# Kernel optimization log

Measured on AMD Instinct MI355X. Metric: run time of the kernel, lower is better.

## Reference

```python
import jax, jax.numpy as jnp
import numpy as np

B, T, F, H, D = 64, 256, 128, 8, 256
E = F * H          # MHA embed dim = input_dim * feat_dim = 1024
HEADS = 4
HD = E // HEADS


def setup_inputs() -> dict:
    key = jax.random.key(0)
    ks = jax.random.split(key, 12)
    def w(k, shape, fan_in):
        return (jax.random.normal(k, shape, jnp.float32) / np.float32(np.sqrt(fan_in)))
    z = lambda *s: jnp.zeros(s, jnp.float32)
    return {
        "x": jax.random.normal(ks[0], (B, T, F), jnp.float32),
        # input_attn MLP: Linear(F, F//4) -> GELU -> Linear(F//4, F) -> Sigmoid
        "attn_w1": w(ks[1], (F, F // 4), F), "attn_b1": z(F // 4),
        "attn_w2": w(ks[2], (F // 4, F), F // 4), "attn_b2": z(F),
        # bank of F tiny GRUs (input=1, hidden=H), stacked along feature axis
        "W_ih": w(ks[3], (F, 3 * H), 1),        # input weight per feature (input size 1)
        "W_hh": w(ks[4], (F, 3 * H, H), H),
        "b_ih": z(F, 3 * H), "b_hh": z(F, 3 * H),
        # MultiheadAttention(E, 4 heads)
        "in_proj_w": w(ks[5], (E, 3 * E), E), "in_proj_b": z(3 * E),
        "mha_out_w": w(ks[6], (E, E), E), "mha_out_b": z(E),
        # out_proj: Linear(E, D)
        "outp_w": w(ks[7], (E, D), E), "outp_b": z(D),
        # FFN: Linear(D, 2D) -> GELU -> Linear(2D, D)
        "ffn_w1": w(ks[8], (D, 2 * D), D), "ffn_b1": z(2 * D),
        "ffn_w2": w(ks[9], (2 * D, D), 2 * D), "ffn_b2": z(D),
    }


def _forward(x, attn_w1, attn_b1, attn_w2, attn_b2,
             W_ih, W_hh, b_ih, b_hh,
             in_proj_w, in_proj_b, mha_out_w, mha_out_b,
             outp_w, outp_b, ffn_w1, ffn_b1, ffn_w2, ffn_b2):
    gelu = lambda v: jax.nn.gelu(v, approximate=False)
    bs, ts, _ = x.shape
    # feature gating (dropout layers are identity in eval mode)
    input_attn = jax.nn.sigmoid(gelu(x @ attn_w1 + attn_b1) @ attn_w2 + attn_b2)  # [B,T,F]
    xg = x * input_attn

    # fused bank of F independent GRUs (input size 1, hidden H), scanned over time
    def step(h, xt):  # h: [B,F,H], xt: [B,F]
        gi = xt[..., None] * W_ih + b_ih                       # [B,F,3H]
        gh = jnp.einsum('bfh,fgh->bfg', h, W_hh) + b_hh        # [B,F,3H]
        ir, iz, inn = jnp.split(gi, 3, axis=-1)
        hr, hz, hn = jnp.split(gh, 3, axis=-1)
        r = jax.nn.sigmoid(ir + hr)
        zg = jax.nn.sigmoid(iz + hz)
        n = jnp.tanh(inn + r * hn)
        h_new = (1.0 - zg) * n + zg * h
        return h_new, h_new

    h0 = jnp.zeros((bs, F, H), x.dtype)
    _, ys = jax.lax.scan(step, h0, jnp.moveaxis(xg, 1, 0))     # ys: [T,B,F,H]
    out = jnp.moveaxis(ys, 0, 1).reshape(bs, ts, E)            # [B,T,E]

    # self-attention (eval: no dropout)
    qkv = out @ in_proj_w + in_proj_b                          # [B,T,3E]
    q, k, v = jnp.split(qkv, 3, axis=-1)
    hsplit = lambda t: t.reshape(bs, ts, HEADS, HD)
    q, k, v = hsplit(q), hsplit(k), hsplit(v)
    scores = jnp.einsum('bqhd,bkhd->bhqk', q, k) / np.float32(np.sqrt(HD))
    attn = jax.nn.softmax(scores, axis=-1)
    ctx = jnp.einsum('bhqk,bkhd->bqhd', attn, v).reshape(bs, ts, E)
    mha_out = ctx @ mha_out_w + mha_out_b

    h1 = mha_out @ outp_w + outp_b                             # [B,T,D]
    ffn = gelu(h1 @ ffn_w1 + ffn_b1) @ ffn_w2 + ffn_b2
    y = h1 + ffn
    feature_importance = input_attn.sum(-1)                    # [B,T]
    return y, feature_importance, input_attn


def reference(x, attn_w1, attn_b1, attn_w2, attn_b2,
              W_ih, W_hh, b_ih, b_hh,
              in_proj_w, in_proj_b, mha_out_w, mha_out_b,
              outp_w, outp_b, ffn_w1, ffn_b1, ffn_w2, ffn_b2):
    return _forward(x, attn_w1, attn_b1, attn_w2, attn_b2,
                    W_ih, W_hh, b_ih, b_hh,
                    in_proj_w, in_proj_b, mha_out_w, mha_out_b,
                    outp_w, outp_b, ffn_w1, ffn_b1, ffn_w2, ffn_b2)
```

## Files before the change

kernel.cpp:

```cpp
#include <hip/hip_runtime.h>
#include <hip/hip_bf16.h>
#include <math.h>

#define B_  64
#define T_  256
#define F_  128
#define H_  8
#define E_  1024
#define NH_ 4
#define HD_ 256
#define D_  256

#define OFF_Y_  0L
#define OFF_FI_ 4194304L
#define OFF_IA_ 4210688L

typedef unsigned short u16;
typedef unsigned int   u32;
typedef short bf16x8 __attribute__((ext_vector_type(8)));
typedef float f32x4  __attribute__((ext_vector_type(4)));

__device__ __forceinline__ float bf2f(u16 u) {
  union { u32 u; float f; } x; x.u = ((u32)u) << 16; return x.f;
}
__device__ __forceinline__ u16 f2bf(float f) {
  union { float f; u32 u; } x; x.f = f;
  u32 r = (x.u + 0x7fffu + ((x.u >> 16) & 1u)) >> 16;
  return (u16)r;
}
__device__ __forceinline__ float gelu_exact(float v) {
  return 0.5f * v * (1.f + erff(v * 0.70710678118654752f));
}
__device__ __forceinline__ float sigmoidf_(float v) {
  return 1.f / (1.f + __expf(-v));
}
__device__ __forceinline__ float ldv(const void* p, long i, bool isf) {
  return isf ? ((const float*)p)[i] : bf2f(((const u16*)p)[i]);
}
__device__ __forceinline__ void stv(void* p, long i, float v, bool isf) {
  if (isf) ((float*)p)[i] = v;
  else ((u16*)p)[i] = f2bf(v);
}
__device__ __forceinline__ void gld16(void* lds, const void* g) {
  __builtin_amdgcn_global_load_lds(
      (const __attribute__((address_space(1))) u32*)g,
      (__attribute__((address_space(3))) u32*)lds, 16, 0, 0);
}

__global__ void detect_dtype(const u16* __restrict__ x, u32* __restrict__ flag) {
  if (threadIdx.x == 0 && blockIdx.x == 0) {
    int good = 0;
    for (int i = 0; i < 512; ++i) {
      u16 v = x[i];
      int e = (v >> 7) & 0xFF;
      if (v == 0 || (e >= 100 && e <= 140)) ++good;
    }
    *flag = (good >= 450) ? 0u : 1u;
  }
}

__global__ __launch_bounds__(256)
void convert_in(const void* __restrict__ src, u16* __restrict__ dst, int n,
                const u32* __restrict__ flag) {
  const bool isf = (*flag != 0);
  int i = blockIdx.x * 256 + threadIdx.x;
  if (i < n) dst[i] = isf ? f2bf(((const float*)src)[i]) : ((const u16*)src)[i];
}

__global__ void transpose_cvt(const void* __restrict__ in, u16* __restrict__ out,
                              int R, int C, const u32* __restrict__ flag) {
  const bool isf = (*flag != 0);
  __shared__ float t[32][33];
  const int c0 = blockIdx.x * 32, r0 = blockIdx.y * 32;
  const int tx = threadIdx.x, ty = threadIdx.y;
  for (int i = ty; i < 32; i += 8)
    t[i][tx] = ldv(in, (long)(r0 + i) * C + c0 + tx, isf);
  __syncthreads();
  for (int i = ty; i < 32; i += 8)
    out[(long)(c0 + i) * R + r0 + tx] = f2bf(t[tx][i]);
}

__global__ __launch_bounds__(128)
void input_mlp2(const void* __restrict__ x,
                const void* __restrict__ w1, const void* __restrict__ b1,
                const void* __restrict__ w2, const void* __restrict__ b2,
                const u32* __restrict__ flag,
                u16* __restrict__ xg, void* __restrict__ dout) {
  const bool isf = (*flag != 0);
  const long row = blockIdx.x;
  const int tid = threadIdx.x;
  __shared__ float xr[F_];
  __shared__ float hid[32];
  __shared__ float red[2];
  float xv = ldv(x, row * F_ + tid, isf);
  xr[tid] = xv;
  __syncthreads();
  if (tid < 32) {
    float s = ldv(b1, tid, isf);
    for (int f = 0; f < F_; ++f) s += xr[f] * ldv(w1, f * 32 + tid, isf);
    hid[tid] = gelu_exact(s);
  }
  __syncthreads();
  float s = ldv(b2, tid, isf);
  #pragma unroll 8
  for (int j = 0; j < 32; ++j) s += hid[j] * ldv(w2, j * F_ + tid, isf);
  float ia = sigmoidf_(s);
  stv(dout, OFF_IA_ + row * F_ + tid, ia, isf);
  xg[row * F_ + tid] = f2bf(ia * xv);
  float v = ia;
  for (int o = 32; o > 0; o >>= 1) v += __shfl_down(v, o);
  if ((tid & 63) == 0) red[tid >> 6] = v;
  __syncthreads();
  if (tid == 0) stv(dout, OFF_FI_ + row, red[0] + red[1], isf);
}

__global__ __launch_bounds__(256)
void gru_scan4(const u16* __restrict__ xg, const void* __restrict__ W_ih,
               const void* __restrict__ W_hh, const void* __restrict__ b_ih,
               const void* __restrict__ b_hh, const u32* __restrict__ flag,
               u16* __restrict__ gruo) {
  const bool isf = (*flag != 0);
  const int tid = threadIdx.x;
  const int ric = tid >> 3;
  const int j   = tid & 7;
  const int rec = blockIdx.x * 32 + ric;
  const int b = rec >> 7, f = rec & 127;
  __shared__ __align__(16) float hbuf[32][8];
  float whr[8], whz[8], whn[8];
  #pragma unroll
  for (int k = 0; k < 8; ++k) {
    whr[k] = ldv(W_hh, (long)f * 192 + j * 8 + k, isf);
    whz[k] = ldv(W_hh, (long)f * 192 + (8 + j) * 8 + k, isf);
    whn[k] = ldv(W_hh, (long)f * 192 + (16 + j) * 8 + k, isf);
  }
  const float wir = ldv(W_ih, f * 24 + j, isf);
  const float wiz = ldv(W_ih, f * 24 + 8 + j, isf);
  const float win = ldv(W_ih, f * 24 + 16 + j, isf);
  const float cbr = ldv(b_ih, f * 24 + j, isf) + ldv(b_hh, f * 24 + j, isf);
  const float cbz = ldv(b_ih, f * 24 + 8 + j, isf) + ldv(b_hh, f * 24 + 8 + j, isf);
  const float bin_ = ldv(b_ih, f * 24 + 16 + j, isf);
  const float bhn_ = ldv(b_hh, f * 24 + 16 + j, isf);
  float h[8];
  #pragma unroll
  for (int k = 0; k < 8; ++k) h[k] = 0.f;
  const u16* xp = xg + (long)b * T_ * F_ + f;
  u16* op = gruo + (long)b * T_ * E_ + f * 8 + j;
  float xv = bf2f(xp[0]);
  for (int t = 0; t < T_; ++t) {
    float xn = (t + 1 < T_) ? bf2f(xp[(t + 1) * F_]) : 0.f;
    float ar = fmaf(xv, wir, cbr);
    float az = fmaf(xv, wiz, cbz);
    float an = bhn_;
    #pragma unroll
    for (int k = 0; k < 8; ++k) {
      ar = fmaf(h[k], whr[k], ar);
      az = fmaf(h[k], whz[k], az);
      an = fmaf(h[k], whn[k], an);
    }
    const float r = sigmoidf_(ar);
    const float z = sigmoidf_(az);
    const float a = fmaf(r, an, fmaf(xv, win, bin_));
    const float e = __expf(2.f * a);
    const float n = 1.f - 2.f / (e + 1.f);
    const float hn = fmaf(z, h[j] - n, n);
    op[(long)t * E_] = f2bf(hn);
    hbuf[ric][j] = hn;
    f32x4 h0 = *(const f32x4*)&hbuf[ric][0];
    f32x4 h1 = *(const f32x4*)&hbuf[ric][4];
    h[0] = h0[0]; h[1] = h0[1]; h[2] = h0[2]; h[3] = h0[3];
    h[4] = h1[0]; h[5] = h1[1]; h[6] = h1[2]; h[7] = h1[3];
    xv = xn;
  }
}

template <int EPI, int COUT>
__global__ __launch_bounds__(256)
void gemm_bt(const u16* __restrict__ A, int lda,
             const u16* __restrict__ Bp, int ldb,
             void* __restrict__ Cg, int ldc,
             const u16* __restrict__ bias, const u16* __restrict__ resid,
             int K, int nbn, const u32* __restrict__ flag) {
  const bool isf = (*flag != 0);
  const int nwg = gridDim.x;
  const int q8 = nwg >> 3, r8 = nwg & 7;
  const int xcd = blockIdx.x & 7, off = blockIdx.x >> 3;
  const int wg = (xcd < r8) ? xcd * (q8 + 1) + off
                            : r8 * (q8 + 1) + (xcd - r8) * q8 + off;
  const int bn = wg % nbn, bm = wg / nbn;
  const int w = threadIdx.x >> 6, lane = threadIdx.x & 63;
  __shared__ __align__(16) u16 As[128 * 64];
  __shared__ __align__(16) u16 Bs[128 * 64];
  const long m0 = (long)bm * 128, n0 = (long)bn * 128;
  const int wm = w >> 1, wn = w & 1;
  const int lr8 = lane >> 3;
  const int csw = ((lane & 7) ^ (lr8 & 7)) * 8;
  f32x4 acc[4][4] = {};
  const int nk = K >> 6;
  const int lr = lane & 15, lq = lane >> 4;
  for (int kt = 0; kt < nk; ++kt) {
    const int k0 = kt << 6;
    __syncthreads();
    #pragma unroll
    for (int c = 0; c < 4; ++c) {
      const int rb = w * 32 + c * 8;
      gld16((char*)As + rb * 128, A + (m0 + rb + lr8) * (long)lda + k0 + csw);
      gld16((char*)Bs + rb * 128, Bp + (n0 + rb + lr8) * (long)ldb + k0 + csw);
    }
    __syncthreads();
    #pragma unroll
    for (int sub = 0; sub < 2; ++sub) {
      const int ch = sub * 4 + lq;
      const int cof = ((ch ^ (lr & 7)) << 3);
      bf16x8 af[4], bfv[4];
      #pragma unroll
      for (int i = 0; i < 4; ++i)
        af[i] = *(const bf16x8*)&As[(wm * 64 + i * 16 + lr) * 64 + cof];
      #pragma unroll
      for (int i = 0; i < 4; ++i)
        bfv[i] = *(const bf16x8*)&Bs[(wn * 64 + i * 16 + lr) * 64 + cof];
      #pragma unroll
      for (int i = 0; i < 4; ++i) {
        #pragma unroll
        for (int j = 0; j < 4; ++j)
          acc[i][j] = __builtin_amdgcn_mfma_f32_16x16x32_bf16(af[i], bfv[j], acc[i][j], 0, 0, 0);
      }
    }
  }
  const int rq = lq * 4;
  #pragma unroll
  for (int j = 0; j < 4; ++j) {
    const long col = n0 + wn * 64 + j * 16 + lr;
    const float bv = (EPI >= 1) ? bf2f(bias[col]) : 0.f;
    #pragma unroll
    for (int i = 0; i < 4; ++i) {
      const long row0 = m0 + wm * 64 + i * 16 + rq;
      #pragma unroll
      for (int q = 0; q < 4; ++q) {
        const long row = row0 + q;
        float v = acc[i][j][q] + bv;
        if (EPI == 2) v = gelu_exact(v);
        if (EPI == 3) v += bf2f(resid[row * (long)ldc + col]);
        if (COUT) stv(Cg, row * (long)ldc + col, v, isf);
        else ((u16*)Cg)[row * (long)ldc + col] = f2bf(v);
      }
    }
  }
}

__global__ __launch_bounds__(256)
void attn_fused(const u16* __restrict__ qkv, u16* __restrict__ ctx) {
  const int z = blockIdx.y, bb = z >> 2, hh = z & 3;
  const int w = threadIdx.x >> 6, lane = threadIdx.x & 63;
  const int tid = threadIdx.x;
  const long t0 = (long)blockIdx.x * 64;
  __shared__ __align__(16) u16 P1[10240];
  __shared__ __align__(16) u16 Pl[64 * 264];
  __shared__ __align__(16) u16 Vt[256 * 40];
  const u16* qb = qkv + (long)bb * T_ * 3 * E_ + hh * HD_;
  const u16* kb = qb + E_;
  const u16* vb = qb + 2 * E_;
  const int rr = lane >> 2, cc = lane & 3;
  const int lr = lane & 15, lq = lane >> 4, lk = lq * 8;
  f32x4 acc[16] = {};
  for (int kt = 0; kt < 8; ++kt) {
    const int k0 = kt * 32;
    __syncthreads();
    gld16((char*)P1 + w * 16 * 64, qb + (t0 + w * 16 + rr) * (3L * E_) + k0 + cc * 8);
    #pragma unroll
    for (int c = 0; c < 4; ++c) {
      const int rb = w * 64 + c * 16;
      gld16((char*)P1 + 4096 + rb * 64, kb + (long)(rb + rr) * (3L * E_) + k0 + cc * 8);
    }
    __syncthreads();
    bf16x8 aq = *(const bf16x8*)&P1[(w * 16 + lr) * 32 + lk];
    #pragma unroll
    for (int nt = 0; nt < 16; ++nt) {
      bf16x8 bk = *(const bf16x8*)&P1[2048 + (nt * 16 + lr) * 32 + lk];
      acc[nt] = __builtin_amdgcn_mfma_f32_16x16x32_bf16(aq, bk, acc[nt], 0, 0, 0);
    }
  }
  #pragma unroll
  for (int q = 0; q < 4; ++q) {
    float mx = -3.4e38f;
    #pragma unroll
    for (int nt = 0; nt < 16; ++nt) mx = fmaxf(mx, acc[nt][q]);
    mx = fmaxf(mx, __shfl_xor(mx, 1));
    mx = fmaxf(mx, __shfl_xor(mx, 2));
    mx = fmaxf(mx, __shfl_xor(mx, 4));
    mx = fmaxf(mx, __shfl_xor(mx, 8));
    float e[16], sum = 0.f;
    #pragma unroll
    for (int nt = 0; nt < 16; ++nt) {
      e[nt] = __expf((acc[nt][q] - mx) * 0.0625f);
      sum += e[nt];
    }
    sum += __shfl_xor(sum, 1);
    sum += __shfl_xor(sum, 2);
    sum += __shfl_xor(sum, 4);
    sum += __shfl_xor(sum, 8);
    const float inv = 1.f / sum;
    const int rowl = w * 16 + lq * 4 + q;
    #pragma unroll
    for (int nt = 0; nt < 16; ++nt)
      Pl[rowl * 264 + nt * 16 + lr] = f2bf(e[nt] * inv);
  }
  f32x4 acc2[16] = {};
  for (int st = 0; st < 8; ++st) {
    const int s0 = st * 32;
    __syncthreads();
    #pragma unroll
    for (int c = 0; c < 4; ++c) {
      const int rb = w * 8 + c * 2;
      gld16((char*)P1 + rb * 512, vb + (s0 + rb + (lane >> 5)) * (3L * E_) + (lane & 31) * 8);
    }
    __syncthreads();
    u16 col[32];
    #pragma unroll
    for (int si = 0; si < 32; ++si) col[si] = P1[si * 256 + tid];
    #pragma unroll
    for (int cq = 0; cq < 4; ++cq)
      *(uint4*)&Vt[tid * 40 + cq * 8] = *(const uint4*)&col[cq * 8];
    __syncthreads();
    bf16x8 pa = *(const bf16x8*)&Pl[(w * 16 + lr) * 264 + s0 + lk];
    #pragma unroll
    for (int nt = 0; nt < 16; ++nt) {
      bf16x8 bv = *(const bf16x8*)&Vt[(nt * 16 + lr) * 40 + lk];
      acc2[nt] = __builtin_amdgcn_mfma_f32_16x16x32_bf16(pa, bv, acc2[nt], 0, 0, 0);
    }
  }
  const int rq = lq * 4;
  #pragma unroll
  for (int nt = 0; nt < 16; ++nt) {
    const int cold = nt * 16 + lr;
    #pragma unroll
    for (int q = 0; q < 4; ++q) {
      const long row = t0 + w * 16 + rq + q;
      ctx[((long)bb * T_ + row) * E_ + hh * HD_ + cold] = f2bf(acc2[nt][q]);
    }
  }
}

extern "C" void kernel_launch(void* const* d_in, const int* in_sizes, int n_in,
                              void* d_out, int out_size, void* d_ws, size_t ws_size,
                              hipStream_t stream) {
  (void)in_sizes; (void)n_in; (void)out_size; (void)ws_size;
  char* ws = (char*)d_ws;
  u16* BIASA = (u16*)(ws + 0);
  u32* FLAG  = (u32*)(ws + 12288);
  u16* wtI   = (u16*)(ws + 65536);
  u16* wtM   = (u16*)(ws + 6356992);
  u16* wtO   = (u16*)(ws + 8454144);
  u16* wtF1  = (u16*)(ws + 8978432);
  u16* wtF2  = (u16*)(ws + 9240576);
  u16* XG    = (u16*)(ws + 9502720);
  u16* GRUO  = (u16*)(ws + 16777216);
  u16* CTX   = GRUO;
  u16* QKV   = (u16*)(ws + 50331648);
  u16* MHA   = (u16*)(ws + 50331648);
  u16* H1    = (u16*)(ws + 83886080);
  u16* FFH   = (u16*)(ws + 92274688);

  detect_dtype<<<1, 64, 0, stream>>>((const u16*)d_in[0], FLAG);

  convert_in<<<12, 256, 0, stream>>>(d_in[10], BIASA + 0,    3072, FLAG);
  convert_in<<<4,  256, 0, stream>>>(d_in[12], BIASA + 3072, 1024, FLAG);
  convert_in<<<1,  256, 0, stream>>>(d_in[14], BIASA + 4096, 256,  FLAG);
  convert_in<<<2,  256, 0, stream>>>(d_in[16], BIASA + 4352, 512,  FLAG);
  convert_in<<<1,  256, 0, stream>>>(d_in[18], BIASA + 4864, 256,  FLAG);

  dim3 tb(32, 8);
  transpose_cvt<<<dim3(3072 / 32, 1024 / 32), tb, 0, stream>>>(d_in[9],  wtI,  1024, 3072, FLAG);
  transpose_cvt<<<dim3(1024 / 32, 1024 / 32), tb, 0, stream>>>(d_in[11], wtM,  1024, 1024, FLAG);
  transpose_cvt<<<dim3(256 / 32, 1024 / 32),  tb, 0, stream>>>(d_in[13], wtO,  1024, 256,  FLAG);
  transpose_cvt<<<dim3(512 / 32, 256 / 32),   tb, 0, stream>>>(d_in[15], wtF1, 256,  512,  FLAG);
  transpose_cvt<<<dim3(256 / 32, 512 / 32),   tb, 0, stream>>>(d_in[17], wtF2, 512,  256,  FLAG);

  input_mlp2<<<B_ * T_, 128, 0, stream>>>(d_in[0], d_in[1], d_in[2], d_in[3], d_in[4],
                                          FLAG, XG, d_out);
  gru_scan4<<<256, 256, 0, stream>>>(XG, d_in[5], d_in[6], d_in[7], d_in[8], FLAG, GRUO);

  gemm_bt<1, 0><<<dim3(128 * 24, 1), 256, 0, stream>>>(GRUO, 1024, wtI, 1024,
      QKV, 3072, BIASA, nullptr, 1024, 24, FLAG);
  attn_fused<<<dim3(4, B_ * NH_), 256, 0, stream>>>(QKV, CTX);
  gemm_bt<1, 0><<<dim3(128 * 8, 1), 256, 0, stream>>>(CTX, 1024, wtM, 1024,
      MHA, 1024, BIASA + 3072, nullptr, 1024, 8, FLAG);
  gemm_bt<1, 0><<<dim3(128 * 2, 1), 256, 0, stream>>>(MHA, 1024, wtO, 1024,
      H1, 256, BIASA + 4096, nullptr, 1024, 2, FLAG);
  gemm_bt<2, 0><<<dim3(128 * 4, 1), 256, 0, stream>>>(H1, 256, wtF1, 256,
      FFH, 512, BIASA + 4352, nullptr, 256, 4, FLAG);
  gemm_bt<3, 1><<<dim3(128 * 2, 1), 256, 0, stream>>>(FFH, 512, wtF2, 512,
      d_out, 256, BIASA + 4864, H1, 512, 2, FLAG);
}
```

Before: 461.3 us.

## Fuse output projection and FFN into one tail kernel; reorder GEMM tiles

Replaces the three tail GEMMs (out-proj, FFN up with GELU, FFN down with residual) with a single kernel that keeps the 32-row H1 and FFN hidden tiles in shared memory. This avoids writing and re-reading the H1 and FFH intermediates through global memory and removes two launches. The weights in the fused kernel are read directly from global memory without LDS staging. The remaining GEMM drops its XCD-aware tile remap for a simple M-major block order. The input MLP's first layer is also split across all 128 threads with a partial-sum reduction instead of using only 32 threads.

```diff
diff --git a/kernel.cpp b/kernel.cpp
--- a/kernel.cpp
+++ b/kernel.cpp
@@ -90,16 +90,24 @@
   const long row = blockIdx.x;
   const int tid = threadIdx.x;
   __shared__ float xr[F_];
+  __shared__ float hid4[4][32];
   __shared__ float hid[32];
   __shared__ float red[2];
   float xv = ldv(x, row * F_ + tid, isf);
   xr[tid] = xv;
   __syncthreads();
-  if (tid < 32) {
-    float s = ldv(b1, tid, isf);
-    for (int f = 0; f < F_; ++f) s += xr[f] * ldv(w1, f * 32 + tid, isf);
-    hid[tid] = gelu_exact(s);
-  }
+  {
+    const int g = tid & 31, part = tid >> 5;
+    const int f0 = part * 32;
+    float s = 0.f;
+    #pragma unroll 8
+    for (int f = 0; f < 32; ++f) s += xr[f0 + f] * ldv(w1, (long)(f0 + f) * 32 + g, isf);
+    hid4[part][g] = s;
+  }
+  __syncthreads();
+  if (tid < 32)
+    hid[tid] = gelu_exact(ldv(b1, tid, isf) + hid4[0][tid] + hid4[1][tid]
+                          + hid4[2][tid] + hid4[3][tid]);
   __syncthreads();
   float s = ldv(b2, tid, isf);
   #pragma unroll 8
@@ -173,20 +181,14 @@
   }
 }
 
-template <int EPI, int COUT>
+template <int EPI>
 __global__ __launch_bounds__(256)
 void gemm_bt(const u16* __restrict__ A, int lda,
              const u16* __restrict__ Bp, int ldb,
-             void* __restrict__ Cg, int ldc,
-             const u16* __restrict__ bias, const u16* __restrict__ resid,
-             int K, int nbn, const u32* __restrict__ flag) {
-  const bool isf = (*flag != 0);
-  const int nwg = gridDim.x;
-  const int q8 = nwg >> 3, r8 = nwg & 7;
-  const int xcd = blockIdx.x & 7, off = blockIdx.x >> 3;
-  const int wg = (xcd < r8) ? xcd * (q8 + 1) + off
-                            : r8 * (q8 + 1) + (xcd - r8) * q8 + off;
-  const int bn = wg % nbn, bm = wg / nbn;
+             u16* __restrict__ Cg, int ldc,
+             const u16* __restrict__ bias,
+             int K, int nbm) {
+  const int bm = blockIdx.x % nbm, bn = blockIdx.x / nbm;
   const int w = threadIdx.x >> 6, lane = threadIdx.x & 63;
   __shared__ __align__(16) u16 As[128 * 64];
   __shared__ __align__(16) u16 Bs[128 * 64];
@@ -235,15 +237,121 @@
     for (int i = 0; i < 4; ++i) {
       const long row0 = m0 + wm * 64 + i * 16 + rq;
       #pragma unroll
+      for (int q = 0; q < 4; ++q)
+        Cg[(row0 + q) * (long)ldc + col] = f2bf(acc[i][j][q] + bv);
+    }
+  }
+}
+
+__global__ __launch_bounds__(256)
+void fused_tail(const u16* __restrict__ MHA,
+                const u16* __restrict__ wtO, const u16* __restrict__ wtF1,
+                const u16* __restrict__ wtF2,
+                const u16* __restrict__ bO, const u16* __restrict__ bF1,
+                const u16* __restrict__ bF2,
+                void* __restrict__ Y, const u32* __restrict__ flag) {
+  const bool isf = (*flag != 0);
+  const int w = threadIdx.x >> 6, lane = threadIdx.x & 63;
+  const long m0 = (long)blockIdx.x * 32;
+  __shared__ __align__(16) u16 Astg[32 * 64];
+  __shared__ __align__(16) u16 h1s[32 * 264];
+  __shared__ __align__(16) u16 ffhs[32 * 520];
+  const int lr = lane & 15, lq = lane >> 4;
+  const int rq = lq * 4;
+  const int srow = w * 8 + (lane >> 3);
+  const int csw = ((lane & 7) ^ ((lane >> 3) & 7)) * 8;
+  f32x4 acc1[2][4] = {};
+  for (int kt = 0; kt < 16; ++kt) {
+    const int k0 = kt << 6;
+    __syncthreads();
+    gld16(&Astg[w * 512], MHA + (m0 + srow) * 1024L + k0 + csw);
+    __syncthreads();
+    #pragma unroll
+    for (int kk = 0; kk < 2; ++kk) {
+      const int ch = kk * 4 + lq;
+      const int cof = ((ch ^ (lr & 7)) << 3);
+      bf16x8 af[2];
+      #pragma unroll
+      for (int i = 0; i < 2; ++i)
+        af[i] = *(const bf16x8*)&Astg[(i * 16 + lr) * 64 + cof];
+      #pragma unroll
+      for (int j = 0; j < 4; ++j) {
+        const int n = w * 64 + j * 16 + lr;
+        bf16x8 bfv = *(const bf16x8*)(wtO + n * 1024L + k0 + kk * 32 + lq * 8);
+        #pragma unroll
+        for (int i = 0; i < 2; ++i)
+          acc1[i][j] = __builtin_amdgcn_mfma_f32_16x16x32_bf16(af[i], bfv, acc1[i][j], 0, 0, 0);
+      }
+    }
+  }
+  __syncthreads();
+  #pragma unroll
+  for (int j = 0; j < 4; ++j) {
+    const int col = w * 64 + j * 16 + lr;
+    const float bv = bf2f(bO[col]);
+    #pragma unroll
+    for (int i = 0; i < 2; ++i)
+      #pragma unroll
+      for (int q = 0; q < 4; ++q)
+        h1s[(i * 16 + rq + q) * 264 + col] = f2bf(acc1[i][j][q] + bv);
+  }
+  __syncthreads();
+  f32x4 acc2[2][8] = {};
+  for (int kt = 0; kt < 8; ++kt) {
+    const int k0 = kt << 5;
+    bf16x8 af[2];
+    #pragma unroll
+    for (int i = 0; i < 2; ++i)
+      af[i] = *(const bf16x8*)&h1s[(i * 16 + lr) * 264 + k0 + lq * 8];
+    #pragma unroll
+    for (int j = 0; j < 8; ++j) {
+      const int n = w * 128 + j * 16 + lr;
+      bf16x8 bfv = *(const bf16x8*)(wtF1 + n * 256L + k0 + lq * 8);
+      #pragma unroll
+      for (int i = 0; i < 2; ++i)
+        acc2[i][j] = __builtin_amdgcn_mfma_f32_16x16x32_bf16(af[i], bfv, acc2[i][j], 0, 0, 0);
+    }
+  }
+  __syncthreads();
+  #pragma unroll
+  for (int j = 0; j < 8; ++j) {
+    const int col = w * 128 + j * 16 + lr;
+    const float bv = bf2f(bF1[col]);
+    #pragma unroll
+    for (int i = 0; i < 2; ++i)
+      #pragma unroll
+      for (int q = 0; q < 4; ++q)
+        ffhs[(i * 16 + rq + q) * 520 + col] = f2bf(gelu_exact(acc2[i][j][q] + bv));
+  }
+  __syncthreads();
+  f32x4 acc3[2][4] = {};
+  for (int kt = 0; kt < 16; ++kt) {
+    const int k0 = kt << 5;
+    bf16x8 af[2];
+    #pragma unroll
+    for (int i = 0; i < 2; ++i)
+      af[i] = *(const bf16x8*)&ffhs[(i * 16 + lr) * 520 + k0 + lq * 8];
+    #pragma unroll
+    for (int j = 0; j < 4; ++j) {
+      const int n = w * 64 + j * 16 + lr;
+      bf16x8 bfv = *(const bf16x8*)(wtF2 + n * 512L + k0 + lq * 8);
+      #pragma unroll
+      for (int i = 0; i < 2; ++i)
+        acc3[i][j] = __builtin_amdgcn_mfma_f32_16x16x32_bf16(af[i], bfv, acc3[i][j], 0, 0, 0);
+    }
+  }
+  #pragma unroll
+  for (int j = 0; j < 4; ++j) {
+    const int col = w * 64 + j * 16 + lr;
+    const float bv = bf2f(bF2[col]);
+    #pragma unroll
+    for (int i = 0; i < 2; ++i)
+      #pragma unroll
       for (int q = 0; q < 4; ++q) {
-        const long row = row0 + q;
-        float v = acc[i][j][q] + bv;
-        if (EPI == 2) v = gelu_exact(v);
-        if (EPI == 3) v += bf2f(resid[row * (long)ldc + col]);
-        if (COUT) stv(Cg, row * (long)ldc + col, v, isf);
-        else ((u16*)Cg)[row * (long)ldc + col] = f2bf(v);
+        const int rl = i * 16 + rq + q;
+        const float v = acc3[i][j][q] + bv + bf2f(h1s[rl * 264 + col]);
+        stv(Y, (m0 + rl) * 256L + col, v, isf);
       }
-    }
   }
 }
 
@@ -357,8 +465,6 @@
   u16* CTX   = GRUO;
   u16* QKV   = (u16*)(ws + 50331648);
   u16* MHA   = (u16*)(ws + 50331648);
-  u16* H1    = (u16*)(ws + 83886080);
-  u16* FFH   = (u16*)(ws + 92274688);
 
   detect_dtype<<<1, 64, 0, stream>>>((const u16*)d_in[0], FLAG);
 
@@ -379,15 +485,11 @@
                                           FLAG, XG, d_out);
   gru_scan4<<<256, 256, 0, stream>>>(XG, d_in[5], d_in[6], d_in[7], d_in[8], FLAG, GRUO);
 
-  gemm_bt<1, 0><<<dim3(128 * 24, 1), 256, 0, stream>>>(GRUO, 1024, wtI, 1024,
-      QKV, 3072, BIASA, nullptr, 1024, 24, FLAG);
+  gemm_bt<1><<<dim3(128 * 24, 1), 256, 0, stream>>>(GRUO, 1024, wtI, 1024,
+      QKV, 3072, BIASA, 1024, 128);
   attn_fused<<<dim3(4, B_ * NH_), 256, 0, stream>>>(QKV, CTX);
-  gemm_bt<1, 0><<<dim3(128 * 8, 1), 256, 0, stream>>>(CTX, 1024, wtM, 1024,
-      MHA, 1024, BIASA + 3072, nullptr, 1024, 8, FLAG);
-  gemm_bt<1, 0><<<dim3(128 * 2, 1), 256, 0, stream>>>(MHA, 1024, wtO, 1024,
-      H1, 256, BIASA + 4096, nullptr, 1024, 2, FLAG);
-  gemm_bt<2, 0><<<dim3(128 * 4, 1), 256, 0, stream>>>(H1, 256, wtF1, 256,
-      FFH, 512, BIASA + 4352, nullptr, 256, 4, FLAG);
-  gemm_bt<3, 1><<<dim3(128 * 2, 1), 256, 0, stream>>>(FFH, 512, wtF2, 512,
-      d_out, 256, BIASA + 4864, H1, 512, 2, FLAG);
-}
+  gemm_bt<1><<<dim3(128 * 8, 1), 256, 0, stream>>>(CTX, 1024, wtM, 1024,
+      MHA, 1024, BIASA + 3072, 1024, 128);
+  fused_tail<<<512, 256, 0, stream>>>(MHA, wtO, wtF1, wtF2,
+      BIASA + 4096, BIASA + 4352, BIASA + 4864, d_out, FLAG);
+}
```

Result: faster. 447.9 us (-2.9%).
